# Optimization experiments

Hardware: AMD Instinct MI355X
Metric: run time of the kernel (lower is better)

Reference implementation:

```python
import jax, jax.numpy as jnp
import numpy as np

N_NODES = 100000
N_EDGES = 1600000
IN_CH = 128
HID_CH = 64   # 2 * out_channels
OUT_CH = 32


def setup_inputs() -> dict:
    key = jax.random.key(0)
    k1, k2, k3, k4, k5, k6 = jax.random.split(key, 6)
    x = jax.random.normal(k1, (N_NODES, IN_CH), dtype=jnp.float32)
    edge_index = jax.random.randint(k2, (2, N_EDGES), 0, N_NODES, dtype=jnp.int32)
    # Glorot-style init like torch.nn.Linear inside GCNConv
    s1 = 1.0 / np.sqrt(IN_CH)
    s2 = 1.0 / np.sqrt(HID_CH)
    W1 = jax.random.uniform(k3, (IN_CH, HID_CH), jnp.float32, -s1, s1)
    b1 = jax.random.uniform(k4, (HID_CH,), jnp.float32, -s1, s1)
    W2 = jax.random.uniform(k5, (HID_CH, OUT_CH), jnp.float32, -s2, s2)
    b2 = jax.random.uniform(k6, (OUT_CH,), jnp.float32, -s2, s2)
    return {"x": x, "edge_index": edge_index, "W1": W1, "b1": b1, "W2": W2, "b2": b2}


def gcn_conv(x, src, dst, W, b, num_nodes):
    # linear transform first (PyG GCNConv): [N, F_in] @ [F_in, F_out]
    h = x @ W
    # symmetric normalization with self-loops: deg counts incoming edges + self-loop
    deg = jax.ops.segment_sum(jnp.ones_like(dst, dtype=h.dtype), dst,
                              num_segments=num_nodes) + 1.0  # +1 for self-loop
    dinv = jnp.where(deg > 0, jax.lax.rsqrt(deg), 0.0)
    norm = dinv[src] * dinv[dst]                      # [E]
    msg = h[src] * norm[:, None]                      # gather + scale, [E, F_out]
    out = jax.ops.segment_sum(msg, dst, num_segments=num_nodes)
    # self-loop contribution: norm = dinv[i]*dinv[i]
    out = out + h * (dinv * dinv)[:, None]
    return out + b


def reference(x, edge_index, W1, b1, W2, b2):
    num_nodes = x.shape[0]
    src, dst = edge_index[0], edge_index[1]
    h = jax.nn.relu(gcn_conv(x, src, dst, W1, b1, num_nodes))
    # F.dropout: identity in eval mode (deterministic reference)
    out = jax.nn.relu(gcn_conv(h, src, dst, W2, b2, num_nodes))
    return out
```

## Files before the change

kernel.cpp:

```cpp
#include <hip/hip_runtime.h>
#include <math.h>

constexpr int BLK = 256;
constexpr int NB_MAX = 256;
constexpr int BSHIFT = 9;
constexpr int BSPAN = 1 << BSHIFT;
constexpr int CAP = 10240;
constexpr int CAP2 = 12800;
constexpr int EPT2 = 16;
constexpr int EPBB = BLK * EPT2;

typedef unsigned short u16;
typedef __attribute__((ext_vector_type(8))) short short8_t;
typedef __attribute__((ext_vector_type(4))) float f32x4;

__device__ __forceinline__ u16 f2bf(float f) {
  union { float f; unsigned int i; } v;
  v.f = f;
  unsigned int r = v.i + 0x7FFF + ((v.i >> 16) & 1);
  return (u16)(r >> 16);
}
__device__ __forceinline__ float bf_lo(unsigned u) {
  union { unsigned int i; float f; } v;
  v.i = u << 16;
  return v.f;
}
__device__ __forceinline__ float bf_hi(unsigned u) {
  union { unsigned int i; float f; } v;
  v.i = u & 0xFFFF0000u;
  return v.f;
}

__global__ void __launch_bounds__(BLK) binpass(const int* __restrict__ src,
                                               const int* __restrict__ dst,
                                               int e, int* __restrict__ bins,
                                               int* __restrict__ tail) {
  __shared__ int lcnt[NB_MAX], gbase[NB_MAX], lcur[NB_MAX];
  const int tid = threadIdx.x;
  lcnt[tid] = 0;
  lcur[tid] = 0;
  __syncthreads();
  const int i0 = blockIdx.x * EPBB;
  int bb[EPT2], pk[EPT2];
#pragma unroll
  for (int k = 0; k < EPT2; k++) {
    int i = i0 + k * BLK + tid;
    if (i < e) {
      int d = dst[i], s = src[i];
      bb[k] = d >> BSHIFT;
      pk[k] = ((d & (BSPAN - 1)) << 23) | s;
      atomicAdd(&lcnt[bb[k]], 1);
    } else {
      bb[k] = -1;
    }
  }
  __syncthreads();
  gbase[tid] = atomicAdd(&tail[tid], lcnt[tid]);
  __syncthreads();
#pragma unroll
  for (int k = 0; k < EPT2; k++) {
    if (bb[k] >= 0) {
      int idx = atomicAdd(&lcur[bb[k]], 1);
      bins[bb[k] * CAP + gbase[bb[k]] + idx] = pk[k];
    }
  }
}

__global__ void __launch_bounds__(BLK) bucket_sort(const int* __restrict__ bins,
                                                   const int* __restrict__ tail,
                                                   unsigned* __restrict__ wdesc,
                                                   int* __restrict__ col,
                                                   float* __restrict__ dinv, int n) {
  __shared__ int hist[BSPAN], lpre[BSPAN], lcur[BSPAN], sd[BLK];
  const int b = blockIdx.x, tid = threadIdx.x;
  const int cnt = tail[b];
  const int base = b * CAP2;
  const int node0 = b << BSHIFT;
  const int nNodes = min(BSPAN, n - node0);
  const int* bin = bins + (size_t)b * CAP;

  hist[tid] = 0; hist[tid + BLK] = 0;
  lcur[tid] = 0; lcur[tid + BLK] = 0;
  __syncthreads();
  for (int j = tid; j < cnt; j += BLK) atomicAdd(&hist[(unsigned)bin[j] >> 23], 1);
  __syncthreads();
  int h0 = hist[2 * tid], h1 = hist[2 * tid + 1];
  int p0 = (h0 + 7) & ~7, p1 = (h1 + 7) & ~7;
  int ts = p0 + p1;
  sd[tid] = ts;
  __syncthreads();
  for (int off = 1; off < BLK; off <<= 1) {
    int t = (tid >= off) ? sd[tid - off] : 0;
    __syncthreads();
    sd[tid] += t;
    __syncthreads();
  }
  int ex = sd[tid] - ts;
  lpre[2 * tid] = ex;
  lpre[2 * tid + 1] = ex + p0;
  __syncthreads();
  for (int d = tid; d < nNodes; d += BLK) {
    int hd = hist[d];
    int begd = base + lpre[d];
    wdesc[node0 + d] = ((unsigned)begd << 10) | (unsigned)((hd + 7) >> 3);
    dinv[node0 + d] = rsqrtf((float)hd + 1.0f);
    int pe = (hd + 7) & ~7;
    for (int t = hd; t < pe; t++) col[begd + t] = n;
  }
  __syncthreads();
  for (int j = tid; j < cnt; j += BLK) {
    int pkv = bin[j];
    int dlo = (unsigned)pkv >> 23;
    int idx = atomicAdd(&lcur[dlo], 1);
    col[base + lpre[dlo] + idx] = pkv & 0x7FFFFF;
  }
}

template <int K, int M>
__global__ void __launch_bounds__(BLK) gemm_mfma(const float* __restrict__ X,
                                                 const float* __restrict__ W,
                                                 const float* __restrict__ dinv,
                                                 u16* __restrict__ G, int n) {
  constexpr int KC = K / 32;
  constexpr int CT = M / 16;
  constexpr int PADK = K + 8;
  __shared__ u16 wt_hi[M][PADK];
  __shared__ u16 wt_lo[M][PADK];
  const int tid = threadIdx.x;
  const int lane = tid & 63;
  const int wv = tid >> 6;

  if (blockIdx.x == 0 && tid < M) G[(size_t)n * M + tid] = 0;

  for (int i = tid; i < K * M; i += BLK) {
    int k = i / M, m = i % M;
    float w = W[i];
    unsigned wb = __float_as_uint(w);
    wt_hi[m][k] = (u16)(wb >> 16);
    wt_lo[m][k] = f2bf(w - __uint_as_float(wb & 0xFFFF0000u));
  }
  __syncthreads();

  const int r16 = lane & 15;
  const int oct = lane >> 4;
  int rowA = blockIdx.x * 64 + wv * 16 + r16;
  if (rowA >= n) rowA = n - 1;

  f32x4 acc[CT];
#pragma unroll
  for (int ct = 0; ct < CT; ct++) acc[ct] = (f32x4){0.f, 0.f, 0.f, 0.f};

#pragma unroll
  for (int kc = 0; kc < KC; kc++) {
    const float* xp = &X[(size_t)rowA * K + kc * 32 + oct * 8];
    float4 v0 = *(const float4*)xp;
    float4 v1 = *(const float4*)(xp + 4);
    float vv[8] = {v0.x, v0.y, v0.z, v0.w, v1.x, v1.y, v1.z, v1.w};
    short8_t ahi, alo;
#pragma unroll
    for (int j = 0; j < 8; j++) {
      unsigned xb = __float_as_uint(vv[j]);
      ahi[j] = (short)(xb >> 16);
      alo[j] = (short)f2bf(vv[j] - __uint_as_float(xb & 0xFFFF0000u));
    }
#pragma unroll
    for (int ct = 0; ct < CT; ct++) {
      short8_t bhi = *(const short8_t*)&wt_hi[ct * 16 + r16][kc * 32 + oct * 8];
      short8_t blo = *(const short8_t*)&wt_lo[ct * 16 + r16][kc * 32 + oct * 8];
      acc[ct] = __builtin_amdgcn_mfma_f32_16x16x32_bf16(ahi, bhi, acc[ct], 0, 0, 0);
      acc[ct] = __builtin_amdgcn_mfma_f32_16x16x32_bf16(alo, bhi, acc[ct], 0, 0, 0);
      acc[ct] = __builtin_amdgcn_mfma_f32_16x16x32_bf16(ahi, blo, acc[ct], 0, 0, 0);
    }
  }

  const int rbase = blockIdx.x * 64 + wv * 16 + oct * 4;
  float dv[4];
#pragma unroll
  for (int r = 0; r < 4; r++) {
    int gr = rbase + r;
    dv[r] = (gr < n) ? dinv[gr] : 0.f;
  }
#pragma unroll
  for (int ct = 0; ct < CT; ct++) {
#pragma unroll
    for (int r = 0; r < 4; r++) {
      int gr = rbase + r;
      if (gr < n) G[(size_t)gr * M + ct * 16 + r16] = f2bf(acc[ct][r] * dv[r]);
    }
  }
}


__global__ void __launch_bounds__(BLK) agg1_kernel(const u16* __restrict__ gs,
                                                   const unsigned* __restrict__ wdesc,
                                                   const int* __restrict__ col,
                                                   const float* __restrict__ dinv,
                                                   const float* __restrict__ bias,
                                                   float* __restrict__ out, int n) {
  const int tid = threadIdx.x;
  const int node = blockIdx.x * 16 + (tid >> 4);
  if (node >= n) return;
  const int cs = tid & 15;
  unsigned w = wdesc[node];
  int beg = (int)(w >> 10), nb = (int)(w & 1023);
  float a0, a1, a2, a3;
  {
    uint2 u = *(const uint2*)&gs[(size_t)node * 64 + cs * 4];
    a0 = bf_lo(u.x); a1 = bf_hi(u.x); a2 = bf_lo(u.y); a3 = bf_hi(u.y);
  }
  for (int i = 0; i < nb; i++) {
    int j = beg + i * 8;
    int4 sA = *(const int4*)&col[j];
    int4 sB = *(const int4*)&col[j + 4];
    uint2 u0 = *(const uint2*)&gs[(size_t)sA.x * 64 + cs * 4];
    uint2 u1 = *(const uint2*)&gs[(size_t)sA.y * 64 + cs * 4];
    uint2 u2 = *(const uint2*)&gs[(size_t)sA.z * 64 + cs * 4];
    uint2 u3 = *(const uint2*)&gs[(size_t)sA.w * 64 + cs * 4];
    uint2 u4 = *(const uint2*)&gs[(size_t)sB.x * 64 + cs * 4];
    uint2 u5 = *(const uint2*)&gs[(size_t)sB.y * 64 + cs * 4];
    uint2 u6 = *(const uint2*)&gs[(size_t)sB.z * 64 + cs * 4];
    uint2 u7 = *(const uint2*)&gs[(size_t)sB.w * 64 + cs * 4];
    a0 += bf_lo(u0.x); a1 += bf_hi(u0.x); a2 += bf_lo(u0.y); a3 += bf_hi(u0.y);
    a0 += bf_lo(u1.x); a1 += bf_hi(u1.x); a2 += bf_lo(u1.y); a3 += bf_hi(u1.y);
    a0 += bf_lo(u2.x); a1 += bf_hi(u2.x); a2 += bf_lo(u2.y); a3 += bf_hi(u2.y);
    a0 += bf_lo(u3.x); a1 += bf_hi(u3.x); a2 += bf_lo(u3.y); a3 += bf_hi(u3.y);
    a0 += bf_lo(u4.x); a1 += bf_hi(u4.x); a2 += bf_lo(u4.y); a3 += bf_hi(u4.y);
    a0 += bf_lo(u5.x); a1 += bf_hi(u5.x); a2 += bf_lo(u5.y); a3 += bf_hi(u5.y);
    a0 += bf_lo(u6.x); a1 += bf_hi(u6.x); a2 += bf_lo(u6.y); a3 += bf_hi(u6.y);
    a0 += bf_lo(u7.x); a1 += bf_hi(u7.x); a2 += bf_lo(u7.y); a3 += bf_hi(u7.y);
  }
  float di = dinv[node];
  float4 bv = *(const float4*)&bias[cs * 4];
  float4 o;
  o.x = a0 * di + bv.x; o.y = a1 * di + bv.y;
  o.z = a2 * di + bv.z; o.w = a3 * di + bv.w;
  o.x = o.x > 0.f ? o.x : 0.f;
  o.y = o.y > 0.f ? o.y : 0.f;
  o.z = o.z > 0.f ? o.z : 0.f;
  o.w = o.w > 0.f ? o.w : 0.f;
  *(float4*)&out[(size_t)node * 64 + cs * 4] = o;
}

__global__ void __launch_bounds__(BLK) agg2_kernel(const u16* __restrict__ gs,
                                                   const unsigned* __restrict__ wdesc,
                                                   const int* __restrict__ col,
                                                   const float* __restrict__ dinv,
                                                   const float* __restrict__ bias,
                                                   float* __restrict__ out, int n) {
  const int tid = threadIdx.x;
  const int node = blockIdx.x * 32 + (tid >> 3);
  if (node >= n) return;
  const int cs = tid & 7;
  unsigned w = wdesc[node];
  int beg = (int)(w >> 10), nb = (int)(w & 1023);
  float a0, a1, a2, a3;
  {
    uint2 u = *(const uint2*)&gs[(size_t)node * 32 + cs * 4];
    a0 = bf_lo(u.x); a1 = bf_hi(u.x); a2 = bf_lo(u.y); a3 = bf_hi(u.y);
  }
  for (int i = 0; i < nb; i++) {
    int j = beg + i * 8;
    int4 sA = *(const int4*)&col[j];
    int4 sB = *(const int4*)&col[j + 4];
    uint2 u0 = *(const uint2*)&gs[(size_t)sA.x * 32 + cs * 4];
    uint2 u1 = *(const uint2*)&gs[(size_t)sA.y * 32 + cs * 4];
    uint2 u2 = *(const uint2*)&gs[(size_t)sA.z * 32 + cs * 4];
    uint2 u3 = *(const uint2*)&gs[(size_t)sA.w * 32 + cs * 4];
    uint2 u4 = *(const uint2*)&gs[(size_t)sB.x * 32 + cs * 4];
    uint2 u5 = *(const uint2*)&gs[(size_t)sB.y * 32 + cs * 4];
    uint2 u6 = *(const uint2*)&gs[(size_t)sB.z * 32 + cs * 4];
    uint2 u7 = *(const uint2*)&gs[(size_t)sB.w * 32 + cs * 4];
    a0 += bf_lo(u0.x); a1 += bf_hi(u0.x); a2 += bf_lo(u0.y); a3 += bf_hi(u0.y);
    a0 += bf_lo(u1.x); a1 += bf_hi(u1.x); a2 += bf_lo(u1.y); a3 += bf_hi(u1.y);
    a0 += bf_lo(u2.x); a1 += bf_hi(u2.x); a2 += bf_lo(u2.y); a3 += bf_hi(u2.y);
    a0 += bf_lo(u3.x); a1 += bf_hi(u3.x); a2 += bf_lo(u3.y); a3 += bf_hi(u3.y);
    a0 += bf_lo(u4.x); a1 += bf_hi(u4.x); a2 += bf_lo(u4.y); a3 += bf_hi(u4.y);
    a0 += bf_lo(u5.x); a1 += bf_hi(u5.x); a2 += bf_lo(u5.y); a3 += bf_hi(u5.y);
    a0 += bf_lo(u6.x); a1 += bf_hi(u6.x); a2 += bf_lo(u6.y); a3 += bf_hi(u6.y);
    a0 += bf_lo(u7.x); a1 += bf_hi(u7.x); a2 += bf_lo(u7.y); a3 += bf_hi(u7.y);
  }
  float di = dinv[node];
  float4 bv = *(const float4*)&bias[cs * 4];
  float4 o;
  o.x = a0 * di + bv.x; o.y = a1 * di + bv.y;
  o.z = a2 * di + bv.z; o.w = a3 * di + bv.w;
  o.x = o.x > 0.f ? o.x : 0.f;
  o.y = o.y > 0.f ? o.y : 0.f;
  o.z = o.z > 0.f ? o.z : 0.f;
  o.w = o.w > 0.f ? o.w : 0.f;
  *(float4*)&out[(size_t)node * 32 + cs * 4] = o;
}


extern "C" void kernel_launch(void* const* d_in, const int* in_sizes, int n_in,
                              void* d_out, int out_size, void* d_ws, size_t ws_size,
                              hipStream_t stream) {
  const float* x = (const float*)d_in[0];
  const int* ei = (const int*)d_in[1];
  const float* W1 = (const float*)d_in[2];
  const float* b1 = (const float*)d_in[3];
  const float* W2 = (const float*)d_in[4];
  const float* b2 = (const float*)d_in[5];

  const int N = in_sizes[0] / 128;
  const int E = in_sizes[1] / 2;
  const int* src = ei;
  const int* dst = ei + E;
  const int nb = (N + BSPAN - 1) >> BSHIFT;

  char* p = (char*)d_ws;
  auto take = [&](size_t bytes) -> char* {
    char* q = p;
    p += (bytes + 255) & ~(size_t)255;
    return q;
  };
  int* bins = (int*)take((size_t)NB_MAX * CAP * 4);
  int* tail = (int*)take(NB_MAX * 4);
  unsigned* wdesc = (unsigned*)take((size_t)N * 4);
  int* col = (int*)take((size_t)nb * CAP2 * 4);
  float* dinv = (float*)take((size_t)N * 4);
  u16* g1 = (u16*)take((size_t)(N + 1) * 64 * 2);
  float* h = (float*)take((size_t)N * 64 * 4);
  u16* g2 = (u16*)take((size_t)(N + 1) * 32 * 2);

  hipMemsetAsync(tail, 0, NB_MAX * 4, stream);

  binpass<<<(E + EPBB - 1) / EPBB, BLK, 0, stream>>>(src, dst, E, bins, tail);
  bucket_sort<<<nb, BLK, 0, stream>>>(bins, tail, wdesc, col, dinv, N);

  gemm_mfma<128, 64><<<(N + 63) / 64, BLK, 0, stream>>>(x, W1, dinv, g1, N);
  agg1_kernel<<<(N + 15) / 16, BLK, 0, stream>>>(g1, wdesc, col, dinv, b1, h, N);
  gemm_mfma<64, 32><<<(N + 63) / 64, BLK, 0, stream>>>(h, W2, dinv, g2, N);
  agg2_kernel<<<(N + 31) / 32, BLK, 0, stream>>>(g2, wdesc, col, dinv, b2, (float*)d_out, N);
}
```

Before: 138.5 us.

## Fuse layer-1 aggregation with layer-2 GEMM via shared-memory tile

Merges the first-layer aggregation kernel and the second GEMM into one kernel. Each block aggregates 64 nodes, applies bias and ReLU, then splits the hidden rows into bf16 hi/lo parts in shared memory and runs MFMA against W2 to write the scaled g2 directly. This removes the fp32 hidden-activation round trip through global memory (write then reread) and one kernel launch. In exchange, each block now handles 64 nodes with 4 serial aggregation passes per thread and uses about 27 KB of shared memory, which may lower occupancy and latency hiding for the gather-bound aggregation.

```diff
diff --git a/kernel.cpp b/kernel.cpp
--- a/kernel.cpp
+++ b/kernel.cpp
@@ -190,55 +190,119 @@
   }
 }
 
-
-__global__ void __launch_bounds__(BLK) agg1_kernel(const u16* __restrict__ gs,
-                                                   const unsigned* __restrict__ wdesc,
-                                                   const int* __restrict__ col,
-                                                   const float* __restrict__ dinv,
-                                                   const float* __restrict__ bias,
-                                                   float* __restrict__ out, int n) {
+__global__ void __launch_bounds__(BLK) agg1_gemm2(const u16* __restrict__ gs,
+                                                  const unsigned* __restrict__ wdesc,
+                                                  const int* __restrict__ col,
+                                                  const float* __restrict__ dinv,
+                                                  const float* __restrict__ b1,
+                                                  const float* __restrict__ W2,
+                                                  u16* __restrict__ G2, int n) {
+  constexpr int PADH = 64 + 8;
+  constexpr int PADK = 64 + 8;
+  __shared__ u16 hs_hi[64][PADH], hs_lo[64][PADH];
+  __shared__ u16 w2_hi[32][PADK], w2_lo[32][PADK];
   const int tid = threadIdx.x;
-  const int node = blockIdx.x * 16 + (tid >> 4);
-  if (node >= n) return;
+  const int lane = tid & 63;
+  const int wv = tid >> 6;
+
+  if (blockIdx.x == 0 && tid < 32) G2[(size_t)n * 32 + tid] = 0;
+
+  for (int i = tid; i < 64 * 32; i += BLK) {
+    int k = i / 32, m = i % 32;
+    float w = W2[i];
+    unsigned wb = __float_as_uint(w);
+    w2_hi[m][k] = (u16)(wb >> 16);
+    w2_lo[m][k] = f2bf(w - __uint_as_float(wb & 0xFFFF0000u));
+  }
+
+  const int grp = tid >> 4;
   const int cs = tid & 15;
-  unsigned w = wdesc[node];
-  int beg = (int)(w >> 10), nb = (int)(w & 1023);
-  float a0, a1, a2, a3;
-  {
-    uint2 u = *(const uint2*)&gs[(size_t)node * 64 + cs * 4];
-    a0 = bf_lo(u.x); a1 = bf_hi(u.x); a2 = bf_lo(u.y); a3 = bf_hi(u.y);
-  }
-  for (int i = 0; i < nb; i++) {
-    int j = beg + i * 8;
-    int4 sA = *(const int4*)&col[j];
-    int4 sB = *(const int4*)&col[j + 4];
-    uint2 u0 = *(const uint2*)&gs[(size_t)sA.x * 64 + cs * 4];
-    uint2 u1 = *(const uint2*)&gs[(size_t)sA.y * 64 + cs * 4];
-    uint2 u2 = *(const uint2*)&gs[(size_t)sA.z * 64 + cs * 4];
-    uint2 u3 = *(const uint2*)&gs[(size_t)sA.w * 64 + cs * 4];
-    uint2 u4 = *(const uint2*)&gs[(size_t)sB.x * 64 + cs * 4];
-    uint2 u5 = *(const uint2*)&gs[(size_t)sB.y * 64 + cs * 4];
-    uint2 u6 = *(const uint2*)&gs[(size_t)sB.z * 64 + cs * 4];
-    uint2 u7 = *(const uint2*)&gs[(size_t)sB.w * 64 + cs * 4];
-    a0 += bf_lo(u0.x); a1 += bf_hi(u0.x); a2 += bf_lo(u0.y); a3 += bf_hi(u0.y);
-    a0 += bf_lo(u1.x); a1 += bf_hi(u1.x); a2 += bf_lo(u1.y); a3 += bf_hi(u1.y);
-    a0 += bf_lo(u2.x); a1 += bf_hi(u2.x); a2 += bf_lo(u2.y); a3 += bf_hi(u2.y);
-    a0 += bf_lo(u3.x); a1 += bf_hi(u3.x); a2 += bf_lo(u3.y); a3 += bf_hi(u3.y);
-    a0 += bf_lo(u4.x); a1 += bf_hi(u4.x); a2 += bf_lo(u4.y); a3 += bf_hi(u4.y);
-    a0 += bf_lo(u5.x); a1 += bf_hi(u5.x); a2 += bf_lo(u5.y); a3 += bf_hi(u5.y);
-    a0 += bf_lo(u6.x); a1 += bf_hi(u6.x); a2 += bf_lo(u6.y); a3 += bf_hi(u6.y);
-    a0 += bf_lo(u7.x); a1 += bf_hi(u7.x); a2 += bf_lo(u7.y); a3 += bf_hi(u7.y);
-  }
-  float di = dinv[node];
-  float4 bv = *(const float4*)&bias[cs * 4];
-  float4 o;
-  o.x = a0 * di + bv.x; o.y = a1 * di + bv.y;
-  o.z = a2 * di + bv.z; o.w = a3 * di + bv.w;
-  o.x = o.x > 0.f ? o.x : 0.f;
-  o.y = o.y > 0.f ? o.y : 0.f;
-  o.z = o.z > 0.f ? o.z : 0.f;
-  o.w = o.w > 0.f ? o.w : 0.f;
-  *(float4*)&out[(size_t)node * 64 + cs * 4] = o;
+#pragma unroll
+  for (int t = 0; t < 4; t++) {
+    const int r = grp + t * 16;
+    const int node = blockIdx.x * 64 + r;
+    float a0 = 0.f, a1 = 0.f, a2 = 0.f, a3 = 0.f;
+    if (node < n) {
+      unsigned w = wdesc[node];
+      int beg = (int)(w >> 10), nb = (int)(w & 1023);
+      {
+        uint2 u = *(const uint2*)&gs[(size_t)node * 64 + cs * 4];
+        a0 = bf_lo(u.x); a1 = bf_hi(u.x); a2 = bf_lo(u.y); a3 = bf_hi(u.y);
+      }
+      for (int i = 0; i < nb; i++) {
+        int j = beg + i * 8;
+        int4 sA = *(const int4*)&col[j];
+        int4 sB = *(const int4*)&col[j + 4];
+        uint2 u0 = *(const uint2*)&gs[(size_t)sA.x * 64 + cs * 4];
+        uint2 u1 = *(const uint2*)&gs[(size_t)sA.y * 64 + cs * 4];
+        uint2 u2 = *(const uint2*)&gs[(size_t)sA.z * 64 + cs * 4];
+        uint2 u3 = *(const uint2*)&gs[(size_t)sA.w * 64 + cs * 4];
+        uint2 u4 = *(const uint2*)&gs[(size_t)sB.x * 64 + cs * 4];
+        uint2 u5 = *(const uint2*)&gs[(size_t)sB.y * 64 + cs * 4];
+        uint2 u6 = *(const uint2*)&gs[(size_t)sB.z * 64 + cs * 4];
+        uint2 u7 = *(const uint2*)&gs[(size_t)sB.w * 64 + cs * 4];
+        a0 += bf_lo(u0.x); a1 += bf_hi(u0.x); a2 += bf_lo(u0.y); a3 += bf_hi(u0.y);
+        a0 += bf_lo(u1.x); a1 += bf_hi(u1.x); a2 += bf_lo(u1.y); a3 += bf_hi(u1.y);
+        a0 += bf_lo(u2.x); a1 += bf_hi(u2.x); a2 += bf_lo(u2.y); a3 += bf_hi(u2.y);
+        a0 += bf_lo(u3.x); a1 += bf_hi(u3.x); a2 += bf_lo(u3.y); a3 += bf_hi(u3.y);
+        a0 += bf_lo(u4.x); a1 += bf_hi(u4.x); a2 += bf_lo(u4.y); a3 += bf_hi(u4.y);
+        a0 += bf_lo(u5.x); a1 += bf_hi(u5.x); a2 += bf_lo(u5.y); a3 += bf_hi(u5.y);
+        a0 += bf_lo(u6.x); a1 += bf_hi(u6.x); a2 += bf_lo(u6.y); a3 += bf_hi(u6.y);
+        a0 += bf_lo(u7.x); a1 += bf_hi(u7.x); a2 += bf_lo(u7.y); a3 += bf_hi(u7.y);
+      }
+      float di = dinv[node];
+      float4 bv = *(const float4*)&b1[cs * 4];
+      a0 = a0 * di + bv.x; a1 = a1 * di + bv.y;
+      a2 = a2 * di + bv.z; a3 = a3 * di + bv.w;
+      a0 = a0 > 0.f ? a0 : 0.f;
+      a1 = a1 > 0.f ? a1 : 0.f;
+      a2 = a2 > 0.f ? a2 : 0.f;
+      a3 = a3 > 0.f ? a3 : 0.f;
+    }
+    float hv[4] = {a0, a1, a2, a3};
+#pragma unroll
+    for (int j = 0; j < 4; j++) {
+      unsigned xb = __float_as_uint(hv[j]);
+      hs_hi[r][cs * 4 + j] = (u16)(xb >> 16);
+      hs_lo[r][cs * 4 + j] = f2bf(hv[j] - __uint_as_float(xb & 0xFFFF0000u));
+    }
+  }
+  __syncthreads();
+
+  const int r16 = lane & 15;
+  const int oct = lane >> 4;
+  const int lrow = wv * 16 + r16;
+  f32x4 acc[2];
+  acc[0] = (f32x4){0.f, 0.f, 0.f, 0.f};
+  acc[1] = (f32x4){0.f, 0.f, 0.f, 0.f};
+#pragma unroll
+  for (int kc = 0; kc < 2; kc++) {
+    short8_t ahi = *(const short8_t*)&hs_hi[lrow][kc * 32 + oct * 8];
+    short8_t alo = *(const short8_t*)&hs_lo[lrow][kc * 32 + oct * 8];
+#pragma unroll
+    for (int ct = 0; ct < 2; ct++) {
+      short8_t bhi = *(const short8_t*)&w2_hi[ct * 16 + r16][kc * 32 + oct * 8];
+      short8_t blo = *(const short8_t*)&w2_lo[ct * 16 + r16][kc * 32 + oct * 8];
+      acc[ct] = __builtin_amdgcn_mfma_f32_16x16x32_bf16(ahi, bhi, acc[ct], 0, 0, 0);
+      acc[ct] = __builtin_amdgcn_mfma_f32_16x16x32_bf16(alo, bhi, acc[ct], 0, 0, 0);
+      acc[ct] = __builtin_amdgcn_mfma_f32_16x16x32_bf16(ahi, blo, acc[ct], 0, 0, 0);
+    }
+  }
+  const int rbase = blockIdx.x * 64 + wv * 16 + oct * 4;
+  float dv[4];
+#pragma unroll
+  for (int r = 0; r < 4; r++) {
+    int gr = rbase + r;
+    dv[r] = (gr < n) ? dinv[gr] : 0.f;
+  }
+#pragma unroll
+  for (int ct = 0; ct < 2; ct++) {
+#pragma unroll
+    for (int r = 0; r < 4; r++) {
+      int gr = rbase + r;
+      if (gr < n) G2[(size_t)gr * 32 + ct * 16 + r16] = f2bf(acc[ct][r] * dv[r]);
+    }
+  }
 }
 
 __global__ void __launch_bounds__(BLK) agg2_kernel(const u16* __restrict__ gs,
@@ -320,7 +384,6 @@
   int* col = (int*)take((size_t)nb * CAP2 * 4);
   float* dinv = (float*)take((size_t)N * 4);
   u16* g1 = (u16*)take((size_t)(N + 1) * 64 * 2);
-  float* h = (float*)take((size_t)N * 64 * 4);
   u16* g2 = (u16*)take((size_t)(N + 1) * 32 * 2);
 
   hipMemsetAsync(tail, 0, NB_MAX * 4, stream);
@@ -329,7 +392,6 @@
   bucket_sort<<<nb, BLK, 0, stream>>>(bins, tail, wdesc, col, dinv, N);
 
   gemm_mfma<128, 64><<<(N + 63) / 64, BLK, 0, stream>>>(x, W1, dinv, g1, N);
-  agg1_kernel<<<(N + 15) / 16, BLK, 0, stream>>>(g1, wdesc, col, dinv, b1, h, N);
-  gemm_mfma<64, 32><<<(N + 63) / 64, BLK, 0, stream>>>(h, W2, dinv, g2, N);
+  agg1_gemm2<<<(N + 63) / 64, BLK, 0, stream>>>(g1, wdesc, col, dinv, b1, W2, g2, N);
   agg2_kernel<<<(N + 31) / 32, BLK, 0, stream>>>(g2, wdesc, col, dinv, b2, (float*)d_out, N);
 }
```

After: 139.0 us. Within noise of the previous version (+0.4%).

## Split layer-1 features into 16-column blocks and aggregate per block

Applied to the files above, without the earlier changes.

The first GEMM now writes its bf16 output as four column-blocked planes of 16 features, each node row 32 bytes, instead of one 128-byte row per node. The layer-1 aggregation runs as four passes over a 2D grid, one per plane, with 4 threads per node instead of 16. The aim is a smaller per-plane gather working set that fits better in cache for the random neighbor reads. In exchange the edge lists and descriptors are re-read four times, and each gathered row is a smaller, less efficient 32-byte access.

```diff
diff --git a/kernel.cpp b/kernel.cpp
--- a/kernel.cpp
+++ b/kernel.cpp
@@ -116,7 +116,7 @@
   }
 }
 
-template <int K, int M>
+template <int K, int M, bool BLK16>
 __global__ void __launch_bounds__(BLK) gemm_mfma(const float* __restrict__ X,
                                                  const float* __restrict__ W,
                                                  const float* __restrict__ dinv,
@@ -130,7 +130,12 @@
   const int lane = tid & 63;
   const int wv = tid >> 6;
 
-  if (blockIdx.x == 0 && tid < M) G[(size_t)n * M + tid] = 0;
+  if (blockIdx.x == 0 && tid < M) {
+    if constexpr (BLK16)
+      G[((size_t)(tid >> 4) * (n + 1) + n) * 16 + (tid & 15)] = 0;
+    else
+      G[(size_t)n * M + tid] = 0;
+  }
 
   for (int i = tid; i < K * M; i += BLK) {
     int k = i / M, m = i % M;
@@ -185,41 +190,48 @@
 #pragma unroll
     for (int r = 0; r < 4; r++) {
       int gr = rbase + r;
-      if (gr < n) G[(size_t)gr * M + ct * 16 + r16] = f2bf(acc[ct][r] * dv[r]);
-    }
-  }
-}
-
-
-__global__ void __launch_bounds__(BLK) agg1_kernel(const u16* __restrict__ gs,
-                                                   const unsigned* __restrict__ wdesc,
-                                                   const int* __restrict__ col,
-                                                   const float* __restrict__ dinv,
-                                                   const float* __restrict__ bias,
-                                                   float* __restrict__ out, int n) {
+      if (gr < n) {
+        u16 val = f2bf(acc[ct][r] * dv[r]);
+        if constexpr (BLK16)
+          G[((size_t)ct * (n + 1) + gr) * 16 + r16] = val;
+        else
+          G[(size_t)gr * M + ct * 16 + r16] = val;
+      }
+    }
+  }
+}
+
+__global__ void __launch_bounds__(BLK) agg1_blk(const u16* __restrict__ gball,
+                                                const unsigned* __restrict__ wdesc,
+                                                const int* __restrict__ col,
+                                                const float* __restrict__ dinv,
+                                                const float* __restrict__ b1,
+                                                float* __restrict__ h, int n) {
   const int tid = threadIdx.x;
-  const int node = blockIdx.x * 16 + (tid >> 4);
+  const int pass = blockIdx.y;
+  const u16* gb = gball + (size_t)pass * (n + 1) * 16;
+  const int node = blockIdx.x * 64 + (tid >> 2);
   if (node >= n) return;
-  const int cs = tid & 15;
+  const int cl = tid & 3;
   unsigned w = wdesc[node];
   int beg = (int)(w >> 10), nb = (int)(w & 1023);
   float a0, a1, a2, a3;
   {
-    uint2 u = *(const uint2*)&gs[(size_t)node * 64 + cs * 4];
+    uint2 u = *(const uint2*)&gb[(size_t)node * 16 + cl * 4];
     a0 = bf_lo(u.x); a1 = bf_hi(u.x); a2 = bf_lo(u.y); a3 = bf_hi(u.y);
   }
   for (int i = 0; i < nb; i++) {
     int j = beg + i * 8;
     int4 sA = *(const int4*)&col[j];
     int4 sB = *(const int4*)&col[j + 4];
-    uint2 u0 = *(const uint2*)&gs[(size_t)sA.x * 64 + cs * 4];
-    uint2 u1 = *(const uint2*)&gs[(size_t)sA.y * 64 + cs * 4];
-    uint2 u2 = *(const uint2*)&gs[(size_t)sA.z * 64 + cs * 4];
-    uint2 u3 = *(const uint2*)&gs[(size_t)sA.w * 64 + cs * 4];
-    uint2 u4 = *(const uint2*)&gs[(size_t)sB.x * 64 + cs * 4];
-    uint2 u5 = *(const uint2*)&gs[(size_t)sB.y * 64 + cs * 4];
-    uint2 u6 = *(const uint2*)&gs[(size_t)sB.z * 64 + cs * 4];
-    uint2 u7 = *(const uint2*)&gs[(size_t)sB.w * 64 + cs * 4];
+    uint2 u0 = *(const uint2*)&gb[(size_t)sA.x * 16 + cl * 4];
+    uint2 u1 = *(const uint2*)&gb[(size_t)sA.y * 16 + cl * 4];
+    uint2 u2 = *(const uint2*)&gb[(size_t)sA.z * 16 + cl * 4];
+    uint2 u3 = *(const uint2*)&gb[(size_t)sA.w * 16 + cl * 4];
+    uint2 u4 = *(const uint2*)&gb[(size_t)sB.x * 16 + cl * 4];
+    uint2 u5 = *(const uint2*)&gb[(size_t)sB.y * 16 + cl * 4];
+    uint2 u6 = *(const uint2*)&gb[(size_t)sB.z * 16 + cl * 4];
+    uint2 u7 = *(const uint2*)&gb[(size_t)sB.w * 16 + cl * 4];
     a0 += bf_lo(u0.x); a1 += bf_hi(u0.x); a2 += bf_lo(u0.y); a3 += bf_hi(u0.y);
     a0 += bf_lo(u1.x); a1 += bf_hi(u1.x); a2 += bf_lo(u1.y); a3 += bf_hi(u1.y);
     a0 += bf_lo(u2.x); a1 += bf_hi(u2.x); a2 += bf_lo(u2.y); a3 += bf_hi(u2.y);
@@ -230,7 +242,7 @@
     a0 += bf_lo(u7.x); a1 += bf_hi(u7.x); a2 += bf_lo(u7.y); a3 += bf_hi(u7.y);
   }
   float di = dinv[node];
-  float4 bv = *(const float4*)&bias[cs * 4];
+  float4 bv = *(const float4*)&b1[pass * 16 + cl * 4];
   float4 o;
   o.x = a0 * di + bv.x; o.y = a1 * di + bv.y;
   o.z = a2 * di + bv.z; o.w = a3 * di + bv.w;
@@ -238,7 +250,7 @@
   o.y = o.y > 0.f ? o.y : 0.f;
   o.z = o.z > 0.f ? o.z : 0.f;
   o.w = o.w > 0.f ? o.w : 0.f;
-  *(float4*)&out[(size_t)node * 64 + cs * 4] = o;
+  *(float4*)&h[(size_t)node * 64 + pass * 16 + cl * 4] = o;
 }
 
 __global__ void __launch_bounds__(BLK) agg2_kernel(const u16* __restrict__ gs,
@@ -319,7 +331,7 @@
   unsigned* wdesc = (unsigned*)take((size_t)N * 4);
   int* col = (int*)take((size_t)nb * CAP2 * 4);
   float* dinv = (float*)take((size_t)N * 4);
-  u16* g1 = (u16*)take((size_t)(N + 1) * 64 * 2);
+  u16* g1b = (u16*)take((size_t)4 * (N + 1) * 16 * 2);
   float* h = (float*)take((size_t)N * 64 * 4);
   u16* g2 = (u16*)take((size_t)(N + 1) * 32 * 2);
 
@@ -328,8 +340,8 @@
   binpass<<<(E + EPBB - 1) / EPBB, BLK, 0, stream>>>(src, dst, E, bins, tail);
   bucket_sort<<<nb, BLK, 0, stream>>>(bins, tail, wdesc, col, dinv, N);
 
-  gemm_mfma<128, 64><<<(N + 63) / 64, BLK, 0, stream>>>(x, W1, dinv, g1, N);
-  agg1_kernel<<<(N + 15) / 16, BLK, 0, stream>>>(g1, wdesc, col, dinv, b1, h, N);
-  gemm_mfma<64, 32><<<(N + 63) / 64, BLK, 0, stream>>>(h, W2, dinv, g2, N);
+  gemm_mfma<128, 64, true><<<(N + 63) / 64, BLK, 0, stream>>>(x, W1, dinv, g1b, N);
+  agg1_blk<<<dim3((N + 63) / 64, 4), BLK, 0, stream>>>(g1b, wdesc, col, dinv, b1, h, N);
+  gemm_mfma<64, 32, false><<<(N + 63) / 64, BLK, 0, stream>>>(h, W2, dinv, g2, N);
   agg2_kernel<<<(N + 31) / 32, BLK, 0, stream>>>(g2, wdesc, col, dinv, b2, (float*)d_out, N);
 }
```

Measured after the change: 158.1 us. +14.2%, slower.
